# Kernel optimization log

Hardware: AMD Instinct MI355X
Metric: run time of the kernel (lower is better)

## Reference

```python
import jax, jax.numpy as jnp
import numpy as np

DIM = 64          # module_dim
K = 3             # module_kernel_size
NQ = 8            # NUM_QUESTION_TOKENS
NM = 3            # num_modules
VOCAB = 50
NANS = 2
B = 256
CNN_W = DIM * DIM * K * K      # 36864
CNN_B = DIM
PROJ_W = 2 * DIM * DIM         # 8192
E1 = DIM + CNN_W               # embedding_dim_1
E2 = DIM + 2 * DIM * DIM       # embedding_dim_2
DN = ('NCHW', 'OIHW', 'NCHW')


def conv2d(x, w, pad):
    return jax.lax.conv_general_dilated(x, w, (1, 1), [(pad, pad), (pad, pad)], dimension_numbers=DN)


def maxpool2(x):
    b, c, h, w = x.shape
    return x.reshape(b, c, h // 2, 2, w // 2, 2).max(axis=(3, 5))


def conv_func(q_rep, lhs, rhs):
    # per-sample hypernetwork conv: weights sliced out of q_rep [B, E1+E2]
    bsz = q_rep.shape[0]
    cw = q_rep[:, :CNN_W].reshape(bsz, DIM, DIM, K, K)
    cb = q_rep[:, CNN_W:CNN_W + CNN_B]
    pw = q_rep[:, CNN_W + CNN_B:CNN_W + CNN_B + PROJ_W].reshape(bsz, DIM, 2 * DIM)
    pb = q_rep[:, CNN_W + CNN_B + PROJ_W:]
    inp = jnp.concatenate([lhs, rhs], axis=1)                       # [B,2D,H,W]
    proj = jnp.einsum('bod,bdhw->bohw', pw, inp) + pb[:, :, None, None]

    def one(x, w, b):  # x [D,H,W], w [D,D,K,K]
        y = jax.lax.conv_general_dilated(x[None], w, (1, 1), [(K // 2, K // 2)] * 2, dimension_numbers=DN)[0]
        return jax.nn.relu(y + b[:, None, None])

    return jax.vmap(one)(proj, cw, cb)                              # [B,D,H,W]


def setup_inputs() -> dict:
    key = jax.random.key(0)
    ks = jax.random.split(key, 16)
    s1 = 1.0 / np.sqrt(DIM * K * K)
    s2 = 1.0 / np.sqrt(2 * DIM)
    flat = 512 * 8 * 8  # classifier_proj_dim * (16/2) * (16/2)
    return {
        'image': jax.random.normal(ks[0], (B, 3, 64, 64), jnp.float32),
        'question': jax.random.randint(ks[1], (B, NQ), 0, VOCAB),
        'emb1': jax.random.uniform(ks[2], (VOCAB, E1), jnp.float32, -s1, s1),
        'emb2': jax.random.uniform(ks[3], (VOCAB, E2), jnp.float32, -s2, s2),
        'alpha': jax.random.normal(ks[4], (NM, NQ), jnp.float32),
        'tau0': jax.random.normal(ks[5], (NM, NM + 1), jnp.float32),
        'tau1': jax.random.normal(ks[6], (NM, NM + 1), jnp.float32),
        'w_s0': jax.random.normal(ks[7], (64, 3, 3, 3), jnp.float32) * np.sqrt(2.0 / (3 * 9)),
        'b_s0': jnp.zeros((64,), jnp.float32),
        'w_s1': jax.random.normal(ks[8], (DIM, 64, 3, 3), jnp.float32) * np.sqrt(2.0 / (64 * 9)),
        'b_s1': jnp.zeros((DIM,), jnp.float32),
        'w_proj': jax.random.normal(ks[9], (512, DIM), jnp.float32) * np.sqrt(2.0 / DIM),
        'b_proj': jnp.zeros((512,), jnp.float32),
        'w_fc1': jax.random.normal(ks[10], (1024, flat), jnp.float32) * np.sqrt(2.0 / flat),
        'b_fc1': jnp.zeros((1024,), jnp.float32),
        'w_fc2': jax.random.normal(ks[11], (NANS, 1024), jnp.float32) * np.sqrt(1.0 / 1024),
        'b_fc2': jnp.zeros((NANS,), jnp.float32),
    }


def reference(image, question, emb1, emb2, alpha, tau0, tau1, w_s0, b_s0, w_s1, b_s1, w_proj, b_proj, w_fc1, b_fc1, w_fc2, b_fc2):
    # stem: conv-relu-maxpool x2 -> [B,D,16,16]
    x = maxpool2(jax.nn.relu(conv2d(image, w_s0, 1) + b_s0[None, :, None, None]))
    x = maxpool2(jax.nn.relu(conv2d(x, w_s1, 1) + b_s1[None, :, None, None]))
    # question embedding gather [B,NQ,E1+E2]
    q = jnp.concatenate([emb1[question], emb2[question]], axis=-1)
    h_prev = jnp.stack([jnp.zeros_like(x), x], axis=1)  # [B,2,D,H,W]
    for i in range(NM):
        a = jax.nn.softmax(alpha[i])
        t0 = jax.nn.softmax(tau0[i, :i + 2])
        t1 = jax.nn.softmax(tau1[i, :i + 2])
        q_rep = jnp.einsum('t,btd->bd', a, q)
        lhs = jnp.einsum('n,bnchw->bchw', t0, h_prev)
        rhs = jnp.einsum('n,bnchw->bchw', t1, h_prev)
        h_i = conv_func(q_rep, lhs, rhs)
        h_prev = jnp.concatenate([h_prev, h_i[:, None]], axis=1)
    h = h_prev[:, -1]
    # classifier: 1x1 proj -> relu -> maxpool2 -> fc -> relu -> fc
    c = jax.nn.relu(jnp.einsum('oc,bchw->bohw', w_proj, h) + b_proj[None, :, None, None])
    c = maxpool2(c)
    f = c.reshape(c.shape[0], -1)
    f = jax.nn.relu(f @ w_fc1.T + b_fc1)
    return f @ w_fc2.T + b_fc2
```

## Files before the change

kernel.cpp:

```cpp
#include <hip/hip_runtime.h>
#include <cstdint>


__global__ void k0_softmax(const float* __restrict__ alpha,
                           const float* __restrict__ tau0,
                           const float* __restrict__ tau1,
                           float* __restrict__ soft) {
  int t = threadIdx.x;
  if (t < 3) {
    float m = -1e30f;
    for (int j = 0; j < 8; j++) m = fmaxf(m, alpha[t*8+j]);
    float e[8]; float s = 0.f;
    #pragma unroll
    for (int j = 0; j < 8; j++) { e[j] = expf(alpha[t*8+j]-m); s += e[j]; }
    #pragma unroll
    for (int j = 0; j < 8; j++) soft[t*8+j] = e[j]/s;
  } else if (t >= 4 && t < 7) {
    int i = t-4; int n = i+2;
    float m = -1e30f;
    for (int j = 0; j < n; j++) m = fmaxf(m, tau0[i*4+j]);
    float e[4]; float s = 0.f;
    for (int j = 0; j < n; j++) { e[j] = expf(tau0[i*4+j]-m); s += e[j]; }
    for (int j = 0; j < 4; j++) soft[24+i*4+j] = (j<n) ? e[j]/s : 0.f;
  } else if (t >= 8 && t < 11) {
    int i = t-8; int n = i+2;
    float m = -1e30f;
    for (int j = 0; j < n; j++) m = fmaxf(m, tau1[i*4+j]);
    float e[4]; float s = 0.f;
    for (int j = 0; j < n; j++) { e[j] = expf(tau1[i*4+j]-m); s += e[j]; }
    for (int j = 0; j < 4; j++) soft[36+i*4+j] = (j<n) ? e[j]/s : 0.f;
  }
}

__global__ __launch_bounds__(256) void kpre_wt(const float* __restrict__ w1,
                                               float* __restrict__ w1t) {
  int i = blockIdx.x*256 + threadIdx.x;
  int oc = i / 576; int rem = i - oc*576; int ic = rem / 9; int tap = rem - ic*9;
  w1t[(ic*9 + tap)*64 + oc] = w1[i];
}

__global__ __launch_bounds__(256) void k1_stem1(
    const float* __restrict__ image, const float* __restrict__ w0,
    const float* __restrict__ b0, float* __restrict__ x1) {
  __shared__ float img[3*66*66];
  __shared__ float wls[64*27];
  __shared__ float bls[64];
  int bx = blockIdx.x;
  int b = bx >> 1, half = bx & 1;
  int t = threadIdx.x;
  for (int i = t; i < 3*66*66; i += 256) img[i] = 0.f;
  for (int i = t; i < 1728; i += 256) wls[i] = w0[i];
  if (t < 64) bls[t] = b0[t];
  __syncthreads();
  const float* ib = image + (size_t)b*3*4096;
  for (int i = t*4; i < 12288; i += 1024) {
    float4 v = *(const float4*)&ib[i];
    int c = i >> 12, r = (i >> 6) & 63, x = i & 63;
    float* dst = &img[c*4356 + (r+1)*66 + (x+1)];
    dst[0]=v.x; dst[1]=v.y; dst[2]=v.z; dst[3]=v.w;
  }
  __syncthreads();
  int py = t >> 3, px0 = (t & 7) * 4;
  float* outb = x1 + ((size_t)b*64 + half*32)*1024;
  for (int oc = 0; oc < 32; oc++) {
    int oco = half*32 + oc;
    float val[2][8];
    #pragma unroll
    for (int r = 0; r < 2; r++)
      #pragma unroll
      for (int c = 0; c < 8; c++) val[r][c] = 0.f;
    #pragma unroll
    for (int ic = 0; ic < 3; ic++) {
      float wn[4][10];
      #pragma unroll
      for (int r = 0; r < 4; r++) {
        #pragma unroll
        for (int c = 0; c < 10; c += 2) {
          float2 v = *(const float2*)&img[ic*4356 + (2*py+r)*66 + 2*px0 + c];
          wn[r][c] = v.x; wn[r][c+1] = v.y;
        }
      }
      const float* wp = &wls[oco*27 + ic*9];
      float w9[9];
      #pragma unroll
      for (int j = 0; j < 9; j++) w9[j] = wp[j];
      #pragma unroll
      for (int dy = 0; dy < 3; dy++)
        #pragma unroll
        for (int dx = 0; dx < 3; dx++) {
          float w = w9[dy*3+dx];
          #pragma unroll
          for (int r = 0; r < 2; r++)
            #pragma unroll
            for (int c = 0; c < 8; c++)
              val[r][c] = fmaf(w, wn[r+dy][c+dx], val[r][c]);
        }
    }
    float bias = bls[oco];
    float4 o4;
    float* po = (float*)&o4;
    #pragma unroll
    for (int c = 0; c < 4; c++) {
      float m = fmaxf(fmaxf(val[0][2*c], val[0][2*c+1]),
                      fmaxf(val[1][2*c], val[1][2*c+1]));
      po[c] = fmaxf(m + bias, 0.f);
    }
    *(float4*)&outb[(size_t)oc*1024 + py*32 + px0] = o4;
  }
}

__global__ __launch_bounds__(256) void k2_stem2(
    const float* __restrict__ x1, const float* __restrict__ w1t,
    const float* __restrict__ b1, float* __restrict__ h1) {
  __shared__ float inp[8*34*34];
  int bx = blockIdx.x;
  int b  = (bx & 7)*32 + ((bx >> 3) & 31);
  int ocb = (bx >> 8) * 16;
  int t = threadIdx.x;
  for (int i = t; i < 9248; i += 256) inp[i] = 0.f;
  int py = t >> 4, px = t & 15;
  float val[16][2][2];
  #pragma unroll
  for (int o = 0; o < 16; o++) { val[o][0][0]=0.f; val[o][0][1]=0.f; val[o][1][0]=0.f; val[o][1][1]=0.f; }
  const float* xb = x1 + (size_t)b*65536;
  for (int icc = 0; icc < 8; icc++) {
    __syncthreads();
    for (int i = t*4; i < 8192; i += 1024) {
      int icl = i >> 10;
      float4 v = *(const float4*)&xb[(size_t)(icc*8+icl)*1024 + (i & 1023)];
      float* dst = &inp[icl*1156 + (((i>>5)&31)+1)*34 + (i&31) + 1];
      dst[0]=v.x; dst[1]=v.y; dst[2]=v.z; dst[3]=v.w;
    }
    __syncthreads();
    for (int icl = 0; icl < 8; icl++) {
      int ic = icc*8 + icl;
      float wn[4][4];
      #pragma unroll
      for (int r = 0; r < 4; r++) {
        float2 v0 = *(const float2*)&inp[icl*1156 + (2*py+r)*34 + 2*px];
        float2 v1 = *(const float2*)&inp[icl*1156 + (2*py+r)*34 + 2*px + 2];
        wn[r][0]=v0.x; wn[r][1]=v0.y; wn[r][2]=v1.x; wn[r][3]=v1.y;
      }
      const float* wrow = w1t + (size_t)ic*576 + ocb;
      #pragma unroll
      for (int tap = 0; tap < 9; tap++) {
        const float4* wp = (const float4*)(wrow + tap*64);
        float4 wv0 = wp[0], wv1 = wp[1], wv2 = wp[2], wv3 = wp[3];
        float w16[16] = {wv0.x,wv0.y,wv0.z,wv0.w, wv1.x,wv1.y,wv1.z,wv1.w,
                         wv2.x,wv2.y,wv2.z,wv2.w, wv3.x,wv3.y,wv3.z,wv3.w};
        int dy = tap / 3, dx = tap - dy*3;
        #pragma unroll
        for (int oc = 0; oc < 16; oc++) {
          float w = w16[oc];
          #pragma unroll
          for (int r = 0; r < 2; r++)
            #pragma unroll
            for (int c = 0; c < 2; c++)
              val[oc][r][c] = fmaf(w, wn[r+dy][c+dx], val[oc][r][c]);
        }
      }
    }
  }
  float* hb = h1 + ((size_t)b*64 + ocb)*256;
  #pragma unroll
  for (int oc = 0; oc < 16; oc++) {
    float m = fmaxf(fmaxf(val[oc][0][0], val[oc][0][1]),
                    fmaxf(val[oc][1][0], val[oc][1][1]));
    hb[(size_t)oc*256 + py*16 + px] = fmaxf(m + b1[ocb+oc], 0.f);
  }
}

__global__ __launch_bounds__(256) void k3_blend(
    const int* __restrict__ question, const float* __restrict__ emb1,
    const float* __restrict__ emb2, const float* __restrict__ soft,
    float* __restrict__ qrep, int iter) {
  int b = blockIdx.y;
  int part = blockIdx.x;
  int t = threadIdx.x;
  int idx[8]; float a[8];
  #pragma unroll
  for (int q = 0; q < 8; q++) { idx[q] = question[b*8+q]; a[q] = soft[iter*8+q]; }
  float* qb = qrep + (size_t)b*45184;
  #pragma unroll
  for (int i = 0; i < 4; i++) {
    int r = i*256 + t;
    int j4 = part*944 + r;
    if (r < 944 && j4 < 11296) {
      int j = j4*4;
      float4 acc = {0.f,0.f,0.f,0.f};
      if (j < 36928) {
        #pragma unroll
        for (int q = 0; q < 8; q++) {
          float4 v = *(const float4*)&emb1[(size_t)idx[q]*36928 + j];
          acc.x = fmaf(a[q], v.x, acc.x); acc.y = fmaf(a[q], v.y, acc.y);
          acc.z = fmaf(a[q], v.z, acc.z); acc.w = fmaf(a[q], v.w, acc.w);
        }
      } else {
        int jj = j - 36928;
        #pragma unroll
        for (int q = 0; q < 8; q++) {
          float4 v = *(const float4*)&emb2[(size_t)idx[q]*8256 + jj];
          acc.x = fmaf(a[q], v.x, acc.x); acc.y = fmaf(a[q], v.y, acc.y);
          acc.z = fmaf(a[q], v.z, acc.z); acc.w = fmaf(a[q], v.w, acc.w);
        }
      }
      *(float4*)&qb[j] = acc;
    }
  }
}

__global__ __launch_bounds__(512) void k4_module(
    const float* __restrict__ qrep, const float* __restrict__ soft,
    const float* __restrict__ h1, const float* __restrict__ h2,
    const float* __restrict__ h3, float* __restrict__ hout, int iter) {
  extern __shared__ float sm[];
  float* inpB0 = sm;
  float* inpB1 = sm + 8192;
  float* pwsB0 = sm + 16384;
  float* pwsB1 = sm + 18432;
  float* ppad  = sm;
  float* cwtB0 = sm + 23040;
  float* cwtB1 = sm + 29184;
  __shared__ float cbpb[128];
  int b = blockIdx.x;
  int t = threadIdx.x;
  int og = t >> 6, pg = t & 63;
  int o8 = og*8, p4 = pg*4;
  int y = pg >> 2, x0 = (pg & 3)*4;
  size_t hb = (size_t)b*16384;
  const float* qb = qrep + (size_t)b*45184;

  if (t < 64) cbpb[t] = qb[36864 + t];
  else if (t < 128) cbpb[t] = qb[45120 + (t - 64)];

  float l1 = soft[24+iter*4+1];
  float l2 = (iter>=1) ? soft[24+iter*4+2] : 0.f;
  float l3 = (iter>=2) ? soft[24+iter*4+3] : 0.f;
  float r1 = soft[36+iter*4+1];
  float r2 = (iter>=1) ? soft[36+iter*4+2] : 0.f;
  float r3 = (iter>=2) ? soft[36+iter*4+3] : 0.f;

  float acc[8][4];
  #pragma unroll
  for (int i = 0; i < 8; i++)
    #pragma unroll
    for (int j = 0; j < 4; j++) acc[i][j] = 0.f;

  auto issueA = [&](int c, float4* v1, float4* v2, float4* v3, float4& pw) {
    #pragma unroll
    for (int p = 0; p < 4; p++) {
      int i4 = t + p*512;
      int dl = i4 >> 6;
      int pix = (i4 & 63) * 4;
      int ch = (c & 1)*32 + dl;
      size_t off = hb + (size_t)ch*256 + pix;
      v1[p] = *(const float4*)&h1[off];
      if (iter >= 1) v2[p] = *(const float4*)&h2[off];
      if (iter >= 2) v3[p] = *(const float4*)&h3[off];
    }
    int o = t >> 3, dq = (t & 7)*4;
    pw = *(const float4*)&qb[36928 + o*128 + c*32 + dq];
  };
  auto writeA = [&](int c, float4* v1, float4* v2, float4* v3, float4& pw,
                    float* inpb, float* pwsb) {
    float c1 = (c >= 2) ? r1 : l1;
    float c2 = (c >= 2) ? r2 : l2;
    float c3 = (c >= 2) ? r3 : l3;
    #pragma unroll
    for (int p = 0; p < 4; p++) {
      int i4 = t + p*512;
      int dl = i4 >> 6;
      int pix = (i4 & 63) * 4;
      float4 v;
      v.x = c1*v1[p].x; v.y = c1*v1[p].y; v.z = c1*v1[p].z; v.w = c1*v1[p].w;
      if (iter >= 1) {
        v.x = fmaf(c2, v2[p].x, v.x); v.y = fmaf(c2, v2[p].y, v.y);
        v.z = fmaf(c2, v2[p].z, v.z); v.w = fmaf(c2, v2[p].w, v.w);
      }
      if (iter >= 2) {
        v.x = fmaf(c3, v3[p].x, v.x); v.y = fmaf(c3, v3[p].y, v.y);
        v.z = fmaf(c3, v3[p].z, v.z); v.w = fmaf(c3, v3[p].w, v.w);
      }
      *(float4*)&inpb[dl*256 + pix] = v;
    }
    int o = t >> 3, dq = (t & 7)*4;
    *(float4*)&pwsb[o*32 + dq] = pw;
  };

  {
    float4 a1[4], a2[4], a3[4], apw;
    issueA(0, a1, a2, a3, apw);
    writeA(0, a1, a2, a3, apw, inpB0, pwsB0);
  }
  __syncthreads();
  #pragma unroll
  for (int c = 0; c < 4; c++) {
    float4 b1v[4], b2v[4], b3v[4], bpw;
    if (c < 3) issueA(c+1, b1v, b2v, b3v, bpw);
    float* inpb = (c & 1) ? inpB1 : inpB0;
    float* pwsb = (c & 1) ? pwsB1 : pwsB0;
    for (int dl = 0; dl < 32; dl++) {
      float w[8];
      #pragma unroll
      for (int oi = 0; oi < 8; oi++) w[oi] = pwsb[(o8+oi)*32 + dl];
      float4 v = *(const float4*)&inpb[dl*256 + p4];
      float vv[4] = {v.x, v.y, v.z, v.w};
      #pragma unroll
      for (int oi = 0; oi < 8; oi++)
        #pragma unroll
        for (int pi = 0; pi < 4; pi++)
          acc[oi][pi] = fmaf(w[oi], vv[pi], acc[oi][pi]);
    }
    __syncthreads();
    if (c < 3) {
      writeA(c+1, b1v, b2v, b3v, bpw, (c & 1) ? inpB0 : inpB1,
             (c & 1) ? pwsB0 : pwsB1);
      __syncthreads();
    }
  }

  float pbv[8];
  #pragma unroll
  for (int oi = 0; oi < 8; oi++) pbv[oi] = cbpb[64 + o8 + oi];
  for (int k = t; k < 23040; k += 512) ppad[k] = 0.f;
  __syncthreads();
  #pragma unroll
  for (int oi = 0; oi < 8; oi++)
    #pragma unroll
    for (int pi = 0; pi < 4; pi++)
      ppad[(o8+oi)*360 + (y+1)*20 + (x0+1) + pi] = acc[oi][pi] + pbv[oi];
  __syncthreads();

  float acc2[8][4];
  #pragma unroll
  for (int i = 0; i < 8; i++)
    #pragma unroll
    for (int j = 0; j < 4; j++) acc2[i][j] = 0.f;

  auto issueB = [&](int icc, float* r) {
    #pragma unroll
    for (int p = 0; p < 9; p++) {
      int i = t + p*512;
      int oc = i / 72;
      int jj = i - oc*72;
      r[p] = qb[oc*576 + icc*72 + jj];
    }
  };
  auto writeB = [&](float* r, float* cwtb) {
    #pragma unroll
    for (int p = 0; p < 9; p++) {
      int i = t + p*512;
      int oc = i / 72;
      int jj = i - oc*72;
      int icl = jj / 9;
      int tap = jj - icl*9;
      cwtb[oc*96 + icl*12 + tap] = r[p];
    }
  };

  {
    float rg[9];
    issueB(0, rg);
    writeB(rg, cwtB0);
  }
  __syncthreads();
  #pragma unroll 1
  for (int icc = 0; icc < 8; icc++) {
    float rn[9];
    if (icc < 7) issueB(icc+1, rn);
    float* cwtb = (icc & 1) ? cwtB1 : cwtB0;
    for (int icl = 0; icl < 8; icl++) {
      int ic = icc*8 + icl;
      float wn[3][6];
      #pragma unroll
      for (int r = 0; r < 3; r++) {
        const float* pr = &ppad[ic*360 + (y+r)*20 + x0];
        float4 aa = *(const float4*)&pr[0];
        float2 bb2 = *(const float2*)&pr[4];
        wn[r][0]=aa.x; wn[r][1]=aa.y; wn[r][2]=aa.z; wn[r][3]=aa.w;
        wn[r][4]=bb2.x; wn[r][5]=bb2.y;
      }
      #pragma unroll
      for (int oi = 0; oi < 8; oi++) {
        const float* wp = &cwtb[(o8+oi)*96 + icl*12];
        float4 wA = *(const float4*)&wp[0];
        float4 wB = *(const float4*)&wp[4];
        float w8v = wp[8];
        float w9[9] = {wA.x,wA.y,wA.z,wA.w, wB.x,wB.y,wB.z,wB.w, w8v};
        #pragma unroll
        for (int dy = 0; dy < 3; dy++)
          #pragma unroll
          for (int dx = 0; dx < 3; dx++) {
            float w = w9[dy*3+dx];
            #pragma unroll
            for (int pi = 0; pi < 4; pi++)
              acc2[oi][pi] = fmaf(w, wn[dy][pi+dx], acc2[oi][pi]);
          }
      }
    }
    __syncthreads();
    if (icc < 7) {
      writeB(rn, (icc & 1) ? cwtB0 : cwtB1);
      __syncthreads();
    }
  }

  float* ho = hout + hb;
  #pragma unroll
  for (int oi = 0; oi < 8; oi++) {
    float cb = cbpb[o8 + oi];
    float4 s0;
    float* p0 = (float*)&s0;
    #pragma unroll
    for (int pi = 0; pi < 4; pi++) p0[pi] = fmaxf(acc2[oi][pi] + cb, 0.f);
    *(float4*)&ho[(size_t)(o8+oi)*256 + y*16 + x0] = s0;
  }
}

__global__ __launch_bounds__(256) void k5_proj(
    const float* __restrict__ h4, const float* __restrict__ wproj,
    const float* __restrict__ bproj, float* __restrict__ f) {
  extern __shared__ float sm[];
  float* hbuf = sm;
  float* wt   = sm + 16384;
  int bx = blockIdx.x;
  int b = (bx & 7)*32 + ((bx >> 3) & 31);
  int ocb = (bx >> 8) * 64;
  int t = threadIdx.x;
  int og = t >> 5, pg = t & 31, o8 = og*8, p8 = pg*8;
  for (int k = t*4; k < 16384; k += 1024)
    *(float4*)&hbuf[k] = *(const float4*)&h4[(size_t)b*16384 + k];
  for (int k = t; k < 4096; k += 256) {
    int ol = k >> 6, c = k & 63;
    wt[c*72 + ol] = wproj[(size_t)(ocb+ol)*64 + c];
  }
  __syncthreads();
  float acc[8][8];
  #pragma unroll
  for (int i = 0; i < 8; i++)
    #pragma unroll
    for (int j = 0; j < 8; j++) acc[i][j] = 0.f;
  for (int d = 0; d < 64; d++) {
    float4 wA = *(const float4*)&wt[d*72 + o8];
    float4 wB = *(const float4*)&wt[d*72 + o8 + 4];
    float4 vA = *(const float4*)&hbuf[d*256 + p8];
    float4 vB = *(const float4*)&hbuf[d*256 + p8 + 4];
    float wv[8] = {wA.x,wA.y,wA.z,wA.w, wB.x,wB.y,wB.z,wB.w};
    float vv[8] = {vA.x,vA.y,vA.z,vA.w, vB.x,vB.y,vB.z,vB.w};
    #pragma unroll
    for (int oi = 0; oi < 8; oi++)
      #pragma unroll
      for (int pi = 0; pi < 8; pi++)
        acc[oi][pi] = fmaf(wv[oi], vv[pi], acc[oi][pi]);
  }
  __syncthreads();
  float bv[8];
  #pragma unroll
  for (int oi = 0; oi < 8; oi++) bv[oi] = bproj[ocb + o8 + oi];
  #pragma unroll
  for (int oi = 0; oi < 8; oi++)
    #pragma unroll
    for (int pi = 0; pi < 8; pi++)
      hbuf[(o8+oi)*256 + p8 + pi] = fmaxf(acc[oi][pi] + bv[oi], 0.f);
  __syncthreads();
  float* fb = f + (size_t)b*32768 + (size_t)ocb*64;
  for (int k = t; k < 4096; k += 256) {
    int oc = k >> 6, pp = k & 63, pyy = pp >> 3, pxx = pp & 7;
    const float* cb_ = &hbuf[oc*256 + pyy*32 + pxx*2];
    float m = fmaxf(fmaxf(cb_[0], cb_[1]), fmaxf(cb_[16], cb_[17]));
    fb[(size_t)oc*64 + pp] = m;
  }
}

__global__ __launch_bounds__(256) void k6_fc1(
    const float* __restrict__ f, const float* __restrict__ w,
    float* __restrict__ part) {
  __shared__ float ab[32*132];
  __shared__ float bb[32*132];
  int bx = blockIdx.x;
  int Mb = (bx & 1)*128;
  int Nb = ((bx >> 1) & 7)*128;
  int Ks = bx >> 4;
  int t = threadIdx.x;
  int og = t >> 4, pg = t & 15, m8 = og*8, n8 = pg*8;
  int kr4 = (t & 7)*4, mr4 = t >> 3;
  float acc[8][8];
  #pragma unroll
  for (int i = 0; i < 8; i++)
    #pragma unroll
    for (int j = 0; j < 8; j++) acc[i][j] = 0.f;
  for (int kc = 0; kc < 64; kc++) {
    int k0 = Ks*2048 + kc*32;
    __syncthreads();
    #pragma unroll
    for (int pass = 0; pass < 4; pass++) {
      int m = pass*32 + mr4;
      float4 av = *(const float4*)&f[(size_t)(Mb+m)*32768 + k0 + kr4];
      float4 bv = *(const float4*)&w[(size_t)(Nb+m)*32768 + k0 + kr4];
      ab[(kr4+0)*132+m] = av.x; ab[(kr4+1)*132+m] = av.y;
      ab[(kr4+2)*132+m] = av.z; ab[(kr4+3)*132+m] = av.w;
      bb[(kr4+0)*132+m] = bv.x; bb[(kr4+1)*132+m] = bv.y;
      bb[(kr4+2)*132+m] = bv.z; bb[(kr4+3)*132+m] = bv.w;
    }
    __syncthreads();
    for (int k = 0; k < 32; k++) {
      float4 aA = *(const float4*)&ab[k*132 + m8];
      float4 aB = *(const float4*)&ab[k*132 + m8 + 4];
      float4 bA = *(const float4*)&bb[k*132 + n8];
      float4 bB = *(const float4*)&bb[k*132 + n8 + 4];
      float a8[8] = {aA.x,aA.y,aA.z,aA.w, aB.x,aB.y,aB.z,aB.w};
      float b8[8] = {bA.x,bA.y,bA.z,bA.w, bB.x,bB.y,bB.z,bB.w};
      #pragma unroll
      for (int mi = 0; mi < 8; mi++)
        #pragma unroll
        for (int ni = 0; ni < 8; ni++)
          acc[mi][ni] = fmaf(a8[mi], b8[ni], acc[mi][ni]);
    }
  }
  float* pb_ = part + (size_t)Ks*262144;
  #pragma unroll
  for (int mi = 0; mi < 8; mi++) {
    float4 s0, s1;
    float* p0 = (float*)&s0; float* p1 = (float*)&s1;
    #pragma unroll
    for (int ni = 0; ni < 4; ni++) p0[ni] = acc[mi][ni];
    #pragma unroll
    for (int ni = 0; ni < 4; ni++) p1[ni] = acc[mi][4+ni];
    *(float4*)&pb_[(size_t)(Mb+m8+mi)*1024 + Nb + n8]     = s0;
    *(float4*)&pb_[(size_t)(Mb+m8+mi)*1024 + Nb + n8 + 4] = s1;
  }
}

__global__ __launch_bounds__(256) void k6b_reduce(
    const float* __restrict__ part, const float* __restrict__ bias,
    float* __restrict__ f2) {
  int j = blockIdx.x*256 + threadIdx.x;
  float s = bias[j & 1023];
  #pragma unroll
  for (int ks = 0; ks < 16; ks++) s += part[(size_t)ks*262144 + j];
  f2[j] = fmaxf(s, 0.f);
}

__global__ __launch_bounds__(256) void k7_fc2(
    const float* __restrict__ f2, const float* __restrict__ w2,
    const float* __restrict__ b2, float* __restrict__ out) {
  __shared__ float r0[256], r1[256];
  int b = blockIdx.x, t = threadIdx.x;
  float s0 = 0.f, s1 = 0.f;
  #pragma unroll
  for (int q = 0; q < 4; q++) {
    int k = q*256 + t;
    float v = f2[(size_t)b*1024 + k];
    s0 = fmaf(v, w2[k], s0);
    s1 = fmaf(v, w2[1024+k], s1);
  }
  r0[t] = s0; r1[t] = s1; __syncthreads();
  for (int s = 128; s > 0; s >>= 1) {
    if (t < s) { r0[t] += r0[t+s]; r1[t] += r1[t+s]; }
    __syncthreads();
  }
  if (t == 0) { out[b*2] = r0[0] + b2[0]; out[b*2+1] = r1[0] + b2[1]; }
}

extern "C" void kernel_launch(void* const* d_in, const int* in_sizes, int n_in,
                              void* d_out, int out_size, void* d_ws, size_t ws_size,
                              hipStream_t stream) {
  const float* image  = (const float*)d_in[0];
  const int*   question = (const int*)d_in[1];
  const float* emb1   = (const float*)d_in[2];
  const float* emb2   = (const float*)d_in[3];
  const float* alpha  = (const float*)d_in[4];
  const float* tau0   = (const float*)d_in[5];
  const float* tau1   = (const float*)d_in[6];
  const float* w_s0   = (const float*)d_in[7];
  const float* b_s0   = (const float*)d_in[8];
  const float* w_s1   = (const float*)d_in[9];
  const float* b_s1   = (const float*)d_in[10];
  const float* w_proj = (const float*)d_in[11];
  const float* b_proj = (const float*)d_in[12];
  const float* w_fc1  = (const float*)d_in[13];
  const float* b_fc1  = (const float*)d_in[14];
  const float* w_fc2  = (const float*)d_in[15];
  const float* b_fc2  = (const float*)d_in[16];
  float* out = (float*)d_out;

  if (ws_size < (size_t)134365440) return;
  float* ws   = (float*)d_ws;
  float* soft = ws;
  float* w1t  = ws + 64;
  float* big  = ws + 36928;
  float* x1   = big;
  float* qrep = big;
  float* f    = big;
  float* part = big + 8388608;
  float* f2   = big + 12582912;
  float* hbuf0 = ws + 36928 + 16777216;
  float* h[4] = { hbuf0, hbuf0 + 4194304, hbuf0 + 8388608, hbuf0 + 12582912 };

  hipFuncSetAttribute(reinterpret_cast<const void*>(k4_module),
                      hipFuncAttributeMaxDynamicSharedMemorySize, 141312);
  hipFuncSetAttribute(reinterpret_cast<const void*>(k5_proj),
                      hipFuncAttributeMaxDynamicSharedMemorySize, 83968);

  k0_softmax<<<1, 64, 0, stream>>>(alpha, tau0, tau1, soft);
  kpre_wt<<<144, 256, 0, stream>>>(w_s1, w1t);
  k1_stem1<<<512, 256, 0, stream>>>(image, w_s0, b_s0, x1);
  k2_stem2<<<1024, 256, 0, stream>>>(x1, w1t, b_s1, h[0]);
  for (int i = 0; i < 3; i++) {
    k3_blend<<<dim3(12, 256), 256, 0, stream>>>(question, emb1, emb2, soft, qrep, i);
    k4_module<<<256, 512, 141312, stream>>>(qrep, soft, h[0], h[1], h[2], h[i+1], i);
  }
  k5_proj<<<2048, 256, 83968, stream>>>(h[3], w_proj, b_proj, f);
  k6_fc1<<<256, 256, 0, stream>>>(f, w_fc1, part);
  k6b_reduce<<<1024, 256, 0, stream>>>(part, b_fc1, f2);
  k7_fc2<<<256, 256, 0, stream>>>(f2, w_fc2, b_fc2, out);
}
```

Measured before the change: 1.373 ms.

## Prefetch fc1 tiles into registers, swizzle LDS, and double split-K

The fc1 GEMM now loads the next K-chunk from global memory into registers while computing on the current LDS tile, so load latency overlaps with FMAs. An XOR-like offset swizzle on LDS columns aims to reduce bank conflicts on both the transposed stores and the float4 reads. Split-K goes from 16 to 32 slices, giving 512 blocks instead of 256 for better CU occupancy. The partial buffer doubles and f2 is relocated into the h buffer region, which adds reduce traffic and a risk of overlapping workspace regions.

After: 1.230 ms. -10.4%, faster.

```diff
diff --git a/kernel.cpp b/kernel.cpp
--- a/kernel.cpp
+++ b/kernel.cpp
@@ -484,30 +484,48 @@
   int t = threadIdx.x;
   int og = t >> 4, pg = t & 15, m8 = og*8, n8 = pg*8;
   int kr4 = (t & 7)*4, mr4 = t >> 3;
+  int wsh = (((t & 7) >> 1) & 1) * 8;
   float acc[8][8];
   #pragma unroll
   for (int i = 0; i < 8; i++)
     #pragma unroll
     for (int j = 0; j < 8; j++) acc[i][j] = 0.f;
-  for (int kc = 0; kc < 64; kc++) {
-    int k0 = Ks*2048 + kc*32;
-    __syncthreads();
+
+  float4 pa[4], pb[4];
+  const float* frow = f + (size_t)(Mb + mr4)*32768 + Ks*1024 + kr4;
+  const float* wrow = w + (size_t)(Nb + mr4)*32768 + Ks*1024 + kr4;
+
+  auto issue = [&](int kc) {
+    int k0 = kc*32;
     #pragma unroll
     for (int pass = 0; pass < 4; pass++) {
-      int m = pass*32 + mr4;
-      float4 av = *(const float4*)&f[(size_t)(Mb+m)*32768 + k0 + kr4];
-      float4 bv = *(const float4*)&w[(size_t)(Nb+m)*32768 + k0 + kr4];
-      ab[(kr4+0)*132+m] = av.x; ab[(kr4+1)*132+m] = av.y;
-      ab[(kr4+2)*132+m] = av.z; ab[(kr4+3)*132+m] = av.w;
-      bb[(kr4+0)*132+m] = bv.x; bb[(kr4+1)*132+m] = bv.y;
-      bb[(kr4+2)*132+m] = bv.z; bb[(kr4+3)*132+m] = bv.w;
-    }
-    __syncthreads();
+      pa[pass] = *(const float4*)&frow[(size_t)pass*32*32768 + k0];
+      pb[pass] = *(const float4*)&wrow[(size_t)pass*32*32768 + k0];
+    }
+  };
+  auto stage = [&]() {
+    #pragma unroll
+    for (int pass = 0; pass < 4; pass++) {
+      int ms = ((pass*32 + mr4 + wsh) & 127);
+      ab[(kr4+0)*132+ms] = pa[pass].x; ab[(kr4+1)*132+ms] = pa[pass].y;
+      ab[(kr4+2)*132+ms] = pa[pass].z; ab[(kr4+3)*132+ms] = pa[pass].w;
+      bb[(kr4+0)*132+ms] = pb[pass].x; bb[(kr4+1)*132+ms] = pb[pass].y;
+      bb[(kr4+2)*132+ms] = pb[pass].z; bb[(kr4+3)*132+ms] = pb[pass].w;
+    }
+  };
+
+  issue(0);
+  stage();
+  __syncthreads();
+  for (int kc = 0; kc < 32; kc++) {
+    if (kc < 31) issue(kc + 1);
+    #pragma unroll 4
     for (int k = 0; k < 32; k++) {
-      float4 aA = *(const float4*)&ab[k*132 + m8];
-      float4 aB = *(const float4*)&ab[k*132 + m8 + 4];
-      float4 bA = *(const float4*)&bb[k*132 + n8];
-      float4 bB = *(const float4*)&bb[k*132 + n8 + 4];
+      int s = ((k >> 3) & 1) * 8;
+      float4 aA = *(const float4*)&ab[k*132 + ((m8 + s) & 127)];
+      float4 aB = *(const float4*)&ab[k*132 + ((m8 + 4 + s) & 127)];
+      float4 bA = *(const float4*)&bb[k*132 + ((n8 + s) & 127)];
+      float4 bB = *(const float4*)&bb[k*132 + ((n8 + 4 + s) & 127)];
       float a8[8] = {aA.x,aA.y,aA.z,aA.w, aB.x,aB.y,aB.z,aB.w};
       float b8[8] = {bA.x,bA.y,bA.z,bA.w, bB.x,bB.y,bB.z,bB.w};
       #pragma unroll
@@ -516,7 +534,13 @@
         for (int ni = 0; ni < 8; ni++)
           acc[mi][ni] = fmaf(a8[mi], b8[ni], acc[mi][ni]);
     }
-  }
+    if (kc < 31) {
+      __syncthreads();
+      stage();
+      __syncthreads();
+    }
+  }
+
   float* pb_ = part + (size_t)Ks*262144;
   #pragma unroll
   for (int mi = 0; mi < 8; mi++) {
@@ -537,7 +561,7 @@
   int j = blockIdx.x*256 + threadIdx.x;
   float s = bias[j & 1023];
   #pragma unroll
-  for (int ks = 0; ks < 16; ks++) s += part[(size_t)ks*262144 + j];
+  for (int ks = 0; ks < 32; ks++) s += part[(size_t)ks*262144 + j];
   f2[j] = fmaxf(s, 0.f);
 }
 
@@ -593,9 +617,9 @@
   float* qrep = big;
   float* f    = big;
   float* part = big + 8388608;
-  float* f2   = big + 12582912;
   float* hbuf0 = ws + 36928 + 16777216;
   float* h[4] = { hbuf0, hbuf0 + 4194304, hbuf0 + 8388608, hbuf0 + 12582912 };
+  float* f2   = hbuf0;
 
   hipFuncSetAttribute(reinterpret_cast<const void*>(k4_module),
                       hipFuncAttributeMaxDynamicSharedMemorySize, 141312);
@@ -611,7 +635,7 @@
     k4_module<<<256, 512, 141312, stream>>>(qrep, soft, h[0], h[1], h[2], h[i+1], i);
   }
   k5_proj<<<2048, 256, 83968, stream>>>(h[3], w_proj, b_proj, f);
-  k6_fc1<<<256, 256, 0, stream>>>(f, w_fc1, part);
+  k6_fc1<<<512, 256, 0, stream>>>(f, w_fc1, part);
   k6b_reduce<<<1024, 256, 0, stream>>>(part, b_fc1, f2);
   k7_fc2<<<256, 256, 0, stream>>>(f2, w_fc2, b_fc2, out);
 }
```
